# Kernel tuning notes

Measured on AMD Instinct MI355X. Metric: run time of the kernel, lower is better.

Reference implementation:

```python
import jax, jax.numpy as jnp
import numpy as np

FACTOR = 5      # ProbAttention sampling factor
NHEAD = 8
LN_EPS = 1e-5


def pos_encoding(L, d):
    pos = np.arange(L, dtype=np.float32)[:, None]
    div = np.exp(np.arange(0, d, 2, dtype=np.float32) * (-np.log(10000.0) / d))
    pe = np.zeros((L, d), np.float32)
    pe[:, 0::2] = np.sin(pos * div)
    pe[:, 1::2] = np.cos(pos * div)
    return jnp.asarray(pe)


def layer_norm(x, s, b):
    mu = x.mean(-1, keepdims=True)
    var = ((x - mu) ** 2).mean(-1, keepdims=True)
    return (x - mu) * jax.lax.rsqrt(var + LN_EPS) * s + b


def prob_attention(x4, key):
    # x4: [B, L, H, D]; self-attention (Q=K=V=x4), mask_flag=False
    B, L, H, D = x4.shape
    q = jnp.transpose(x4, (0, 2, 1, 3))  # [B,H,L,D]
    u = max(1, min(FACTOR * int(np.ceil(np.log(L))), L))  # L_Q == L_K
    # random K-sampling: per-query random subset of keys (shared across B,H)
    idx = jax.random.randint(key, (L, u), 0, L)
    k_s = q[:, :, idx, :]                                # [B,H,L,u,D] irregular gather
    qk_s = jnp.einsum('bhld,bhlsd->bhls', q, k_s)        # [B,H,L,u]
    M = qk_s.max(-1) - qk_s.sum(-1) / L                  # sparsity measure
    _, top = jax.lax.top_k(M, u)                         # [B,H,u] active queries
    q_red = jnp.take_along_axis(q, top[..., None], axis=2)   # [B,H,u,D]
    scale = 1.0 / jnp.sqrt(jnp.float32(D))
    scores = jnp.einsum('bhud,bhkd->bhuk', q_red, q) * scale  # reduced-query scores
    attn = jax.nn.softmax(scores, axis=-1)
    ctx_top = jnp.einsum('bhuk,bhkd->bhud', attn, q)     # V == q here
    # initial context = mean of V (mask_flag=False), scatter top-query results
    ctx = jnp.broadcast_to(q.mean(axis=2, keepdims=True), (B, H, L, D))
    bi = jnp.arange(B)[:, None, None]
    hi = jnp.arange(H)[None, :, None]
    ctx = ctx.at[bi, hi, top].set(ctx_top)
    return jnp.transpose(ctx, (0, 2, 1, 3))  # [B,L,H,D]


def encoder_layer(x4, ln1_s, ln1_b, w1, b1, w2, b2, ln2_s, ln2_b, key):
    B, L, H, D = x4.shape
    new = prob_attention(x4, key)
    x = x4.reshape(B, L, H * D)
    x = layer_norm(x + new.reshape(B, L, H * D), ln1_s, ln1_b)
    # conv1/conv2 with kernel_size=1 == pointwise linears
    y = jax.nn.gelu(jnp.einsum('bld,fd->blf', x, w1) + b1, approximate=False)
    y = jnp.einsum('blf,df->bld', y, w2) + b2
    x = layer_norm(x + y, ln2_s, ln2_b)
    return x.reshape(B, L, H, D)


def distil(x4, factor=2):
    # DistilledAttention: mean-pool over `factor` timesteps (zero-pad to multiple)
    B, L, H, D = x4.shape
    pad = (-L) % factor
    if pad:
        x4 = jnp.pad(x4, ((0, 0), (0, pad), (0, 0), (0, 0)))
    return x4.reshape(B, -1, factor, H, D).mean(axis=2)


def setup_inputs() -> dict:
    key = jax.random.key(0)
    B, L, IN, D, DF, NL = 8, 4096, 64, 512, 2048, 3
    ks = jax.random.split(key, 16)
    s = 0.02
    return {
        'x': jax.random.normal(ks[0], (B, L, IN), jnp.float32),
        'emb_w': jax.random.normal(ks[1], (D, IN), jnp.float32) * s,
        'emb_b': jnp.zeros((D,), jnp.float32),
        'ln1_s': jnp.ones((NL, D), jnp.float32),
        'ln1_b': jnp.zeros((NL, D), jnp.float32),
        'w1': jax.random.normal(ks[2], (NL, DF, D), jnp.float32) * s,
        'b1': jnp.zeros((NL, DF), jnp.float32),
        'w2': jax.random.normal(ks[3], (NL, D, DF), jnp.float32) * s,
        'b2': jnp.zeros((NL, D), jnp.float32),
        'ln2_s': jnp.ones((NL, D), jnp.float32),
        'ln2_b': jnp.zeros((NL, D), jnp.float32),
        'out_w': jax.random.normal(ks[4], (D, D), jnp.float32) * s,
        'out_b': jnp.zeros((D,), jnp.float32),
    }


def reference(x, emb_w, emb_b, ln1_s, ln1_b, w1, b1, w2, b2, ln2_s, ln2_b, out_w, out_b):
    B, L, _ = x.shape
    D = emb_w.shape[0]
    hd = D // NHEAD
    h = jnp.einsum('bli,di->bld', x, emb_w) + emb_b
    h = h + pos_encoding(L, D)[None]
    h = h.reshape(B, L, NHEAD, hd)
    NL = ln1_s.shape[0]
    rkey = jax.random.key(42)  # deterministic ProbSparse sampling
    for i in range(NL):
        h = encoder_layer(h, ln1_s[i], ln1_b[i], w1[i], b1[i], w2[i], b2[i],
                          ln2_s[i], ln2_b[i], jax.random.fold_in(rkey, i))
        if i < NL - 1:
            h = distil(h)
    B2, L2 = h.shape[:2]
    h = h.reshape(B2, L2, D)
    return jnp.einsum('bld,od->blo', h, out_w) + out_b
```

## Files before the change

### kernel.cpp

```cpp
#include <hip/hip_runtime.h>
#include <hip/hip_bf16.h>
#include <math.h>


typedef short short8 __attribute__((ext_vector_type(8)));
typedef float f32x4 __attribute__((ext_vector_type(4)));
typedef unsigned int uint;

__host__ __device__ inline void tf2x32(unsigned k0, unsigned k1,
                                       unsigned x0, unsigned x1,
                                       unsigned& o0, unsigned& o1) {
  unsigned ks2 = k0 ^ k1 ^ 0x1BD11BDAu;
#define TF_R(x, r) x0 += x1; x1 = ((x1 << (r)) | (x1 >> (32 - (r)))); x1 ^= x0;
  x0 += k0; x1 += k1;
  TF_R(x1,13) TF_R(x1,15) TF_R(x1,26) TF_R(x1,6)
  x0 += k1; x1 += ks2 + 1u;
  TF_R(x1,17) TF_R(x1,29) TF_R(x1,16) TF_R(x1,24)
  x0 += ks2; x1 += k0 + 2u;
  TF_R(x1,13) TF_R(x1,15) TF_R(x1,26) TF_R(x1,6)
  x0 += k0; x1 += k1 + 3u;
  TF_R(x1,17) TF_R(x1,29) TF_R(x1,16) TF_R(x1,24)
  x0 += k1; x1 += ks2 + 4u;
  TF_R(x1,13) TF_R(x1,15) TF_R(x1,26) TF_R(x1,6)
  x0 += ks2; x1 += k0 + 5u;
#undef TF_R
  o0 = x0; o1 = x1;
}

__global__ void k_idx(int* __restrict__ idx, unsigned k2a, unsigned k2b,
                      int n, int mask) {
  int j = blockIdx.x * 256 + threadIdx.x;
  if (j >= n) return;
  unsigned o0, o1;
  tf2x32(k2a, k2b, 0u, (unsigned)j, o0, o1);
  idx[j] = (int)((o0 ^ o1) & (unsigned)mask);
}

__global__ void k_pe(float* __restrict__ pe) {
  int t = blockIdx.x * 256 + threadIdx.x;
  int l = t >> 9, d = t & 511;
  double div = exp((double)(d & ~1) * (-9.210340371976184 / 512.0));
  double ang = (double)l * div;
  pe[t] = (float)((d & 1) ? cos(ang) : sin(ang));
}

__global__ __launch_bounds__(256) void k_embed(const float* __restrict__ x,
    const float* __restrict__ W, const float* __restrict__ eb,
    const float* __restrict__ pe, float* __restrict__ out) {
  __shared__ __align__(16) float xs[16][64];
  int r0 = blockIdx.x * 16;
  int t = threadIdx.x;
  ((float4*)&xs[0][0])[t] = ((const float4*)(x + (size_t)r0 * 64))[t];
  __syncthreads();
  int d0 = t, d1 = t + 256;
  float acc0[16], acc1[16];
#pragma unroll
  for (int r = 0; r < 16; r++) { acc0[r] = 0.f; acc1[r] = 0.f; }
  for (int k = 0; k < 64; k++) {
    float w0 = W[d0 * 64 + k], w1 = W[d1 * 64 + k];
#pragma unroll
    for (int r = 0; r < 16; r++) {
      float xv = xs[r][k];
      acc0[r] = fmaf(xv, w0, acc0[r]);
      acc1[r] = fmaf(xv, w1, acc1[r]);
    }
  }
  float eb0 = eb[d0], eb1 = eb[d1];
#pragma unroll
  for (int r = 0; r < 16; r++) {
    int row = r0 + r;
    int l = row & 4095;
    out[(size_t)row * 512 + d0] = acc0[r] + eb0 + pe[(size_t)l * 512 + d0];
    out[(size_t)row * 512 + d1] = acc1[r] + eb1 + pe[(size_t)l * 512 + d1];
  }
}

__global__ __launch_bounds__(256) void k_colmean1(const float* __restrict__ X,
    double* __restrict__ part, int L, int S) {
  int seg = blockIdx.x, bh = blockIdx.y, b = bh >> 3, h = bh & 7;
  int w = threadIdx.x >> 6, d = threadIdx.x & 63;
  int rows = L / S, r0 = seg * rows;
  const float* base = X + (size_t)b * L * 512 + h * 64 + d;
  double s = 0.0;
  for (int l = r0 + w; l < r0 + rows; l += 4) s += (double)base[(size_t)l * 512];
  __shared__ double red[4][64];
  red[w][d] = s;
  __syncthreads();
  if (w == 0)
    part[((size_t)bh * S + seg) * 64 + d] =
        red[0][d] + red[1][d] + red[2][d] + red[3][d];
}

__global__ void k_colmean2(const double* __restrict__ part,
    float* __restrict__ meanq, int L, int S) {
  int bh = blockIdx.x, d = threadIdx.x;
  const double* p = part + (size_t)bh * S * 64 + d;
  double s = 0.0;
  for (int seg = 0; seg < S; seg++) s += p[seg * 64];
  meanq[bh * 64 + d] = (float)(s / (double)L);
}

__global__ __launch_bounds__(256) void k_M(const float* __restrict__ X,
    const int* __restrict__ idx, float* __restrict__ Mout, int L, int Lsh,
    int u, float invL) {
  int w = threadIdx.x >> 6, lane = threadIdx.x & 63;
  int gl = blockIdx.x * 4 + w;
  int l = gl & (L - 1), bh = gl >> Lsh, b = bh >> 3, h = bh & 7;
  const float* Xbh = X + (size_t)b * L * 512 + h * 64;
  __shared__ float qs[4][64];
  qs[w][lane] = Xbh[(size_t)l * 512 + lane];
  __syncthreads();
  const int s16 = lane >> 2, j = lane & 3;
  float4 qv[4];
#pragma unroll
  for (int c = 0; c < 4; c++) qv[c] = *(const float4*)&qs[w][c * 16 + j * 4];
  const int base = l * u;
  int kx[3];
#pragma unroll
  for (int g = 0; g < 3; g++) {
    int s = g * 16 + s16;
    kx[g] = (s < u) ? idx[base + s] : 0;
  }
  float4 kv[3][4];
#pragma unroll
  for (int g = 0; g < 3; g++) {
    const float* row = Xbh + (size_t)kx[g] * 512 + j * 4;
#pragma unroll
    for (int c = 0; c < 4; c++) kv[g][c] = *(const float4*)(row + c * 16);
  }
  float mv = -1e30f, sv = 0.f;
#pragma unroll
  for (int g = 0; g < 3; g++) {
    float pc[4];
#pragma unroll
    for (int c = 0; c < 4; c++) {
      float p = qv[c].x * kv[g][c].x;
      p = fmaf(qv[c].y, kv[g][c].y, p);
      p = fmaf(qv[c].z, kv[g][c].z, p);
      p = fmaf(qv[c].w, kv[g][c].w, p);
      pc[c] = p;
    }
    float d = (pc[0] + pc[1]) + (pc[2] + pc[3]);
    d += __shfl_xor(d, 1);
    d += __shfl_xor(d, 2);
    if (g * 16 + s16 < u) { mv = fmaxf(mv, d); sv += d; }
  }
  for (int off = 4; off < 64; off <<= 1) {
    mv = fmaxf(mv, __shfl_xor(mv, off));
    sv += __shfl_xor(sv, off);
  }
  if (lane == 0) Mout[(size_t)bh * L + l] = mv - sv * invL;
}

__global__ __launch_bounds__(256) void k_topk(const float* __restrict__ M,
    int* __restrict__ top, int L, int u) {
  __shared__ float mv[4096];
  __shared__ float wv[4];
  __shared__ int wi[4];
  __shared__ int bi_s;
  int bh = blockIdx.x, t = threadIdx.x;
  int w = t >> 6, lane = t & 63;
  const float* Mr = M + (size_t)bh * L;
  for (int k = t; k < L; k += 256) mv[k] = Mr[k];
  __syncthreads();
  float lv = -1e30f; int li = 0x7fffffff;
  for (int k = t; k < L; k += 256) {
    float v = mv[k];
    if (v > lv) { lv = v; li = k; }
  }
  for (int it = 0; it < u; it++) {
    float v = lv; int i = li;
#pragma unroll
    for (int off = 1; off < 64; off <<= 1) {
      float v2 = __shfl_xor(v, off); int i2 = __shfl_xor(i, off);
      if (v2 > v || (v2 == v && i2 < i)) { v = v2; i = i2; }
    }
    if (lane == 0) { wv[w] = v; wi[w] = i; }
    __syncthreads();
    if (t == 0) {
      float bv = wv[0]; int bi = wi[0];
#pragma unroll
      for (int jj = 1; jj < 4; jj++) {
        if (wv[jj] > bv || (wv[jj] == bv && wi[jj] < bi)) { bv = wv[jj]; bi = wi[jj]; }
      }
      top[bh * u + it] = bi;
      mv[bi] = -1e30f;
      bi_s = bi;
    }
    __syncthreads();
    int bi = bi_s;
    if ((bi & 255) == t) {
      lv = -1e30f; li = 0x7fffffff;
      for (int k = t; k < L; k += 256) {
        float v = mv[k];
        if (v > lv) { lv = v; li = k; }
      }
    }
  }
}

__global__ __launch_bounds__(256) void k_scores(const float* __restrict__ X,
    const int* __restrict__ top, float* __restrict__ S, int L, int u) {
  __shared__ __align__(16) float ktT[64][68];
  __shared__ __align__(16) float qred[48][64];
  int bh = blockIdx.y, b = bh >> 3, h = bh & 7;
  int k0 = blockIdx.x * 64;
  int t = threadIdx.x;
  const float* Xbh = X + (size_t)b * L * 512 + h * 64;
#pragma unroll
  for (int it = 0; it < 4; it++) {
    int lin = t + it * 256;
    int kk = lin >> 4, fi = lin & 15;
    float4 v = *(const float4*)(Xbh + (size_t)(k0 + kk) * 512 + fi * 4);
    ktT[fi * 4 + 0][kk] = v.x; ktT[fi * 4 + 1][kk] = v.y;
    ktT[fi * 4 + 2][kk] = v.z; ktT[fi * 4 + 3][kk] = v.w;
  }
#pragma unroll
  for (int it = 0; it < 3; it++) {
    int lin = t + it * 256;
    int ur = lin >> 4, fi = lin & 15;
    if (ur < u) {
      int row = top[bh * u + ur];
      *(float4*)(&qred[ur][fi * 4]) = *(const float4*)(Xbh + (size_t)row * 512 + fi * 4);
    } else if (ur < 48) {
      *(float4*)(&qred[ur][fi * 4]) = make_float4(0.f, 0.f, 0.f, 0.f);
    }
  }
  __syncthreads();
  int xq = t & 15, y = t >> 4;
  float acc[3][4];
#pragma unroll
  for (int j = 0; j < 3; j++)
#pragma unroll
    for (int e = 0; e < 4; e++) acc[j][e] = 0.f;
  for (int d = 0; d < 64; d++) {
    float4 kv = *(const float4*)(&ktT[d][xq * 4]);
#pragma unroll
    for (int j = 0; j < 3; j++) {
      float qv = qred[y * 3 + j][d];
      acc[j][0] = fmaf(qv, kv.x, acc[j][0]);
      acc[j][1] = fmaf(qv, kv.y, acc[j][1]);
      acc[j][2] = fmaf(qv, kv.z, acc[j][2]);
      acc[j][3] = fmaf(qv, kv.w, acc[j][3]);
    }
  }
#pragma unroll
  for (int j = 0; j < 3; j++) {
    int ur = y * 3 + j;
    if (ur < u) {
      float4 o = make_float4(acc[j][0] * 0.125f, acc[j][1] * 0.125f,
                             acc[j][2] * 0.125f, acc[j][3] * 0.125f);
      *(float4*)(S + ((size_t)(bh * u + ur)) * L + k0 + xq * 4) = o;
    }
  }
}

__global__ __launch_bounds__(256) void k_smstat(const float* __restrict__ S,
    float* __restrict__ MX, double* __restrict__ INV, int L, int u) {
  int ur = blockIdx.x, bh = blockIdx.y;
  const float* Srow = S + ((size_t)(bh * u + ur)) * L;
  int t = threadIdx.x;
  __shared__ float rm[256];
  __shared__ double rs[256];
  float m = -1e30f;
  for (int k = t; k < L; k += 256) m = fmaxf(m, Srow[k]);
  rm[t] = m; __syncthreads();
  for (int off = 128; off; off >>= 1) {
    if (t < off) rm[t] = fmaxf(rm[t], rm[t + off]);
    __syncthreads();
  }
  float mx = rm[0];
  double s = 0.0;
  for (int k = t; k < L; k += 256) s += (double)expf(Srow[k] - mx);
  rs[t] = s; __syncthreads();
  for (int off = 128; off; off >>= 1) {
    if (t < off) rs[t] += rs[t + off];
    __syncthreads();
  }
  if (t == 0) { MX[bh * 48 + ur] = mx; INV[bh * 48 + ur] = 1.0 / rs[0]; }
}

#define PVSEG 8
__global__ __launch_bounds__(256) void k_pv(const float* __restrict__ X,
    const float* __restrict__ S, const float* __restrict__ MX,
    float* __restrict__ P2, int L, int u) {
  __shared__ __align__(16) float xs[32][64];
  __shared__ __align__(16) float wsm[32][52];
  int seg = blockIdx.x, bh = blockIdx.y, b = bh >> 3, h = bh & 7;
  int t = threadIdx.x, w = t >> 6, lane = t & 63;
  int rows = L / PVSEG, l0 = seg * rows;
  const float* Xb = X + (size_t)b * L * 512 + h * 64;
  int li = lane & 31, par = lane >> 5;
  const float* Sp[6]; float mxl[6]; int val[6];
#pragma unroll
  for (int jj = 0; jj < 6; jj++) {
    int ur = w * 12 + par + jj * 2;
    val[jj] = (ur < u);
    Sp[jj] = S + (size_t)(bh * u + (val[jj] ? ur : 0)) * L + l0 + li;
    mxl[jj] = val[jj] ? MX[bh * 48 + ur] : 0.f;
  }
  float acc[12];
#pragma unroll
  for (int j = 0; j < 12; j++) acc[j] = 0.f;
  int xr = t >> 4, xf = t & 15;
  for (int c = 0; c < rows; c += 32) {
    __syncthreads();
    *(float4*)&xs[xr][xf * 4] =
        *(const float4*)(Xb + (size_t)(l0 + c + xr) * 512 + xf * 4);
    *(float4*)&xs[16 + xr][xf * 4] =
        *(const float4*)(Xb + (size_t)(l0 + c + 16 + xr) * 512 + xf * 4);
#pragma unroll
    for (int jj = 0; jj < 6; jj++) {
      float e = val[jj] ? expf(Sp[jj][c] - mxl[jj]) : 0.f;
      wsm[li][w * 12 + par + jj * 2] = e;
    }
    __syncthreads();
#pragma unroll 2
    for (int l = 0; l < 32; l++) {
      float xv = xs[l][lane];
      float4 w0 = *(const float4*)&wsm[l][w * 12];
      float4 w1 = *(const float4*)&wsm[l][w * 12 + 4];
      float4 w2 = *(const float4*)&wsm[l][w * 12 + 8];
      acc[0]  = fmaf(w0.x, xv, acc[0]);  acc[1]  = fmaf(w0.y, xv, acc[1]);
      acc[2]  = fmaf(w0.z, xv, acc[2]);  acc[3]  = fmaf(w0.w, xv, acc[3]);
      acc[4]  = fmaf(w1.x, xv, acc[4]);  acc[5]  = fmaf(w1.y, xv, acc[5]);
      acc[6]  = fmaf(w1.z, xv, acc[6]);  acc[7]  = fmaf(w1.w, xv, acc[7]);
      acc[8]  = fmaf(w2.x, xv, acc[8]);  acc[9]  = fmaf(w2.y, xv, acc[9]);
      acc[10] = fmaf(w2.z, xv, acc[10]); acc[11] = fmaf(w2.w, xv, acc[11]);
    }
  }
  float* P = P2 + ((size_t)(bh * PVSEG + seg) * 48 + w * 12) * 64 + lane;
#pragma unroll
  for (int j = 0; j < 12; j++) P[j * 64] = acc[j];
}

__global__ __launch_bounds__(256) void k_pvred(const float* __restrict__ P2,
    const double* __restrict__ INV, const int* __restrict__ top,
    float* __restrict__ A, char* __restrict__ FLG, int L, int u) {
  int bh = blockIdx.x, b = bh >> 3, h = bh & 7;
  const float* Pb = P2 + (size_t)bh * PVSEG * 48 * 64;
  for (int e = threadIdx.x; e < u * 64; e += 256) {
    int ur = e >> 6, d = e & 63;
    const float* p = Pb + ur * 64 + d;
    const int st = 48 * 64;
    double s = ((double)p[0] + (double)p[st]) +
               ((double)p[2 * st] + (double)p[3 * st]) +
               ((double)p[4 * st] + (double)p[5 * st]) +
               ((double)p[6 * st] + (double)p[7 * st]);
    double tot = s * INV[bh * 48 + ur];
    int row = top[bh * u + ur];
    A[((size_t)b * L + row) * 512 + h * 64 + d] = (float)tot;
    if (d == 0) FLG[(size_t)bh * L + row] = 1;
  }
}

__global__ __launch_bounds__(256) void k_ln1(float* __restrict__ X,
    const float* __restrict__ A, const char* __restrict__ FLG,
    const float* __restrict__ meanq, const float* __restrict__ gs,
    const float* __restrict__ gb, int L, int Lsh) {
  int w = threadIdx.x >> 6, lane = threadIdx.x & 63;
  int row = blockIdx.x * 4 + w;
  int b = row >> Lsh, l = row & (L - 1);
  float* xr = X + (size_t)row * 512;
  const float* ar = A + (size_t)row * 512;
  const float* mq = meanq + b * 512;
  const char* fg = FLG + ((size_t)b * 8) * L + l;
  float v[8]; double s = 0.0, s2 = 0.0;
#pragma unroll
  for (int i = 0; i < 8; i++) {
    int d = lane + i * 64;
    float ctx = fg[(size_t)i * L] ? ar[d] : mq[d];
    float val = xr[d] + ctx;
    v[i] = val; s += (double)val; s2 += (double)val * (double)val;
  }
  for (int off = 32; off; off >>= 1) { s += __shfl_xor(s, off); s2 += __shfl_xor(s2, off); }
  double mu = s * (1.0 / 512.0);
  double var = s2 * (1.0 / 512.0) - mu * mu;
  float rsd = (float)(1.0 / sqrt(var + 1e-5));
  float muf = (float)mu;
#pragma unroll
  for (int i = 0; i < 8; i++) {
    int d = lane + i * 64;
    xr[d] = (v[i] - muf) * rsd * gs[d] + gb[d];
  }
}

__global__ __launch_bounds__(256) void k_ln2(const float* __restrict__ X,
    const float* __restrict__ Y2, const float* __restrict__ gs,
    const float* __restrict__ gb, float* __restrict__ out, int pool) {
  int w = threadIdx.x >> 6, lane = threadIdx.x & 63;
  int orow = blockIdx.x * 4 + w;
  float o[8] = {0.f,0.f,0.f,0.f,0.f,0.f,0.f,0.f};
  int reps = pool ? 2 : 1;
  for (int p = 0; p < reps; p++) {
    int row = pool ? (orow * 2 + p) : orow;
    const float* xr = X + (size_t)row * 512;
    const float* yr = Y2 + (size_t)row * 512;
    float v[8]; double s = 0.0, s2 = 0.0;
#pragma unroll
    for (int i = 0; i < 8; i++) {
      float val = xr[lane + i * 64] + yr[lane + i * 64];
      v[i] = val; s += (double)val; s2 += (double)val * (double)val;
    }
    for (int off = 32; off; off >>= 1) { s += __shfl_xor(s, off); s2 += __shfl_xor(s2, off); }
    double mu = s * (1.0 / 512.0);
    double var = s2 * (1.0 / 512.0) - mu * mu;
    float rsd = (float)(1.0 / sqrt(var + 1e-5));
    float muf = (float)mu;
#pragma unroll
    for (int i = 0; i < 8; i++)
      o[i] += (v[i] - muf) * rsd * gs[lane + i * 64] + gb[lane + i * 64];
  }
  float sc = pool ? 0.5f : 1.0f;
#pragma unroll
  for (int i = 0; i < 8; i++)
    out[(size_t)orow * 512 + lane + i * 64] = o[i] * sc;
}


__device__ inline unsigned bsplit(float x, float y, float& rx, float& ry) {
  union { __hip_bfloat162 h; unsigned u; } c;
  c.h = __float22bfloat162_rn(make_float2(x, y));
  rx = x - __uint_as_float(c.u << 16);
  ry = y - __uint_as_float(c.u & 0xffff0000u);
  return c.u;
}

__device__ inline void split2u(float4 v0, float4 v1, uint4& H, uint4& M) {
  float r[8]; float d0, d1;
  H.x = bsplit(v0.x, v0.y, r[0], r[1]);
  H.y = bsplit(v0.z, v0.w, r[2], r[3]);
  H.z = bsplit(v1.x, v1.y, r[4], r[5]);
  H.w = bsplit(v1.z, v1.w, r[6], r[7]);
  M.x = bsplit(r[0], r[1], d0, d1);
  M.y = bsplit(r[2], r[3], d0, d1);
  M.z = bsplit(r[4], r[5], d0, d1);
  M.w = bsplit(r[6], r[7], d0, d1);
}

__global__ void k_splitX(const float* __restrict__ X, char* __restrict__ P,
                         int K, int total8) {
  int f = blockIdx.x * 256 + threadIdx.x;
  if (f >= total8) return;
  int k8 = f % (K >> 3), m = f / (K >> 3);
  int k = k8 * 8;
  const float* src = X + (size_t)m * K + k;
  float4 v0 = *(const float4*)(src);
  float4 v1 = *(const float4*)(src + 4);
  uint4 H, Md;
  split2u(v0, v1, H, Md);
  size_t psz = (size_t)total8 * 16;
  size_t off = ((size_t)(m >> 4) * (K >> 5) + (k >> 5)) * 1024
             + (size_t)(((k >> 3) & 3) * 256 + (m & 15) * 16);
  *(uint4*)(P + off) = H;
  *(uint4*)(P + psz + off) = Md;
}

__device__ __forceinline__ void async16(void* lds, const void* g) {
  __builtin_amdgcn_global_load_lds(
      (const __attribute__((address_space(1))) uint*)g,
      (__attribute__((address_space(3))) uint*)lds, 16, 0, 0);
}

template <int MT, int GELU, int PLANES_OUT>
__global__ __launch_bounds__(256) void k_gemm6(const char* __restrict__ AP,
    const char* __restrict__ BP, const float* __restrict__ bias,
    void* __restrict__ Cout, int N, int K) {
  __shared__ __align__(16) char lds[(MT * 2 + 16) * 1024];
  const int t = threadIdx.x;
  const int w = t >> 6, lane = t & 63;
  const int bx = blockIdx.x, by = blockIdx.y;
  const int quad = lane >> 4, rit = lane & 15;
  const int Mrows = gridDim.y * (MT * 16);
  const size_t psA = (size_t)Mrows * K * 2;
  const size_t psB = (size_t)N * K * 2;
  const int KB = K >> 5;
  char* ldsA = lds;
  char* ldsB = lds + MT * 2 * 1024;
  const int wm = (w >> 1) * (MT / 2), wn = (w & 1) * 4;
  f32x4 acc[MT / 2][4];
#pragma unroll
  for (int i = 0; i < MT / 2; i++)
#pragma unroll
    for (int j = 0; j < 4; j++) acc[i][j] = (f32x4){0.f, 0.f, 0.f, 0.f};
  for (int kt = 0; kt < KB; kt++) {
#pragma unroll
    for (int r = 0; r < MT / 2; r++) {
      int q = w + 4 * r;
      int p = q / MT, tt = q % MT;
      async16(ldsA + (p * MT + tt) * 1024,
              AP + p * psA + ((size_t)(by * MT + tt) * KB + kt) * 1024 + lane * 16);
    }
#pragma unroll
    for (int r = 0; r < 4; r++) {
      int q = w + 4 * r;
      int p = q >> 3, tt = q & 7;
      async16(ldsB + (p * 8 + tt) * 1024,
              BP + p * psB + ((size_t)(bx * 8 + tt) * KB + kt) * 1024 + lane * 16);
    }
    __syncthreads();
    short8 af[2][MT / 2];
#pragma unroll
    for (int p = 0; p < 2; p++)
#pragma unroll
      for (int mi = 0; mi < MT / 2; mi++)
        af[p][mi] = *(const short8*)(ldsA + (p * MT + wm + mi) * 1024 + lane * 16);
#pragma unroll
    for (int ni = 0; ni < 4; ni++) {
      const char* bb = ldsB + (wn + ni) * 1024 + lane * 16;
      short8 bh = *(const short8*)(bb);
      short8 bm = *(const short8*)(bb + 8192);
#pragma unroll
      for (int mi = 0; mi < MT / 2; mi++) {
        f32x4 c = acc[mi][ni];
        c = __builtin_amdgcn_mfma_f32_16x16x32_bf16(af[0][mi], bh, c, 0, 0, 0);
        c = __builtin_amdgcn_mfma_f32_16x16x32_bf16(af[0][mi], bm, c, 0, 0, 0);
        c = __builtin_amdgcn_mfma_f32_16x16x32_bf16(af[1][mi], bh, c, 0, 0, 0);
        acc[mi][ni] = c;
      }
    }
    __syncthreads();
  }
  const int n0 = bx * 128, m_base = by * (MT * 16);
  if (!PLANES_OUT) {
    float* C = (float*)Cout;
#pragma unroll
    for (int mi = 0; mi < MT / 2; mi++) {
      const int gr0 = m_base + (wm + mi) * 16 + quad * 4;
#pragma unroll
      for (int ni = 0; ni < 4; ni++) {
        const int gc = n0 + (wn + ni) * 16 + rit;
        const float bia = bias[gc];
#pragma unroll
        for (int e = 0; e < 4; e++) {
          float v = acc[mi][ni][e] + bia;
          if (GELU) v = 0.5f * v * (1.0f + erff(v * 0.7071067811865476f));
          C[(size_t)(gr0 + e) * N + gc] = v;
        }
      }
    }
  } else {
    char* CP = (char*)Cout;
    const size_t psC = (size_t)Mrows * N * 2;
    float* lf = (float*)lds;
    for (int h = 0; h < 2; h++) {
      __syncthreads();
      if ((w & 1) == h) {
#pragma unroll
        for (int ni = 0; ni < 4; ni++) {
          const float bia = bias[n0 + h * 64 + ni * 16 + rit];
#pragma unroll
          for (int mi = 0; mi < MT / 2; mi++) {
            const int ml0 = (wm + mi) * 16 + quad * 4;
#pragma unroll
            for (int e = 0; e < 4; e++) {
              float v = acc[mi][ni][e] + bia;
              if (GELU) v = 0.5f * v * (1.0f + erff(v * 0.7071067811865476f));
              lf[(ml0 + e) * 64 + ni * 16 + rit] = v;
            }
          }
        }
      }
      __syncthreads();
#pragma unroll
      for (int it = 0; it < (MT * 16 * 8) / 256; it++) {
        int p = it * 256 + t;
        int ml = p >> 3, n8 = p & 7;
        float4 v0 = *(const float4*)&lf[ml * 64 + n8 * 8];
        float4 v1 = *(const float4*)&lf[ml * 64 + n8 * 8 + 4];
        uint4 H, Md;
        split2u(v0, v1, H, Md);
        int mg = m_base + ml, kg = n0 + h * 64 + n8 * 8;
        size_t off = ((size_t)(mg >> 4) * (N >> 5) + (kg >> 5)) * 1024
                   + (size_t)(((kg >> 3) & 3) * 256 + (mg & 15) * 16);
        *(uint4*)(CP + off) = H;
        *(uint4*)(CP + psC + off) = Md;
      }
    }
  }
}

extern "C" void kernel_launch(void* const* d_in, const int* in_sizes, int n_in,
                              void* d_out, int out_size, void* d_ws, size_t ws_size,
                              hipStream_t stream) {
  const float* x     = (const float*)d_in[0];
  const float* emb_w = (const float*)d_in[1];
  const float* emb_b = (const float*)d_in[2];
  const float* ln1_s = (const float*)d_in[3];
  const float* ln1_b = (const float*)d_in[4];
  const float* w1    = (const float*)d_in[5];
  const float* b1    = (const float*)d_in[6];
  const float* w2    = (const float*)d_in[7];
  const float* b2    = (const float*)d_in[8];
  const float* ln2_s = (const float*)d_in[9];
  const float* ln2_b = (const float*)d_in[10];
  const float* out_w = (const float*)d_in[11];
  const float* out_b = (const float*)d_in[12];
  float* outp = (float*)d_out;

  char* ws = (char*)d_ws;
  if (ws_size < (212ULL << 20)) return;
  float* PE    = (float*)(ws);
  char*  W1S   = ws;
  float* BUF[3] = { (float*)(ws + (8ULL << 20)),
                    (float*)(ws + (72ULL << 20)),
                    (float*)(ws + (136ULL << 20)) };
  char*  W2S   = ws + (200ULL << 20);
  float* MB    = (float*)(ws + (206ULL << 20));
  int*   IDX   = (int*)  (ws + (207ULL << 20));
  int*   TOP   = (int*)  (ws + (208ULL << 20));
  float* MEANQ = (float*)(ws + (208ULL << 20) + (64 << 10));
  float* MXB   = (float*)(ws + (208ULL << 20) + (128 << 10));
  double* INVB = (double*)(ws + (208ULL << 20) + (192 << 10));
  double* PART = (double*)(ws + (209ULL << 20));
  char*  FLG   = ws + (210ULL << 20);

  k_pe<<<4096 * 512 / 256, 256, 0, stream>>>(PE);
  k_embed<<<(8 * 4096) / 16, 256, 0, stream>>>(x, emb_w, emb_b, PE, BUF[0]);

  const int Ls[3] = {4096, 2048, 1024};
  const int Lshs[3] = {12, 11, 10};
  const int us[3] = {45, 40, 35};
  int xi = 0, ai = 1, yi = 2;
  for (int layer = 0; layer < 3; layer++) {
    const int L = Ls[layer], u = us[layer];
    float* X = BUF[xi]; float* A = BUF[ai]; float* Y = BUF[yi];

    k_splitX<<<(2048 * 512 / 8) / 256, 256, 0, stream>>>(
        w1 + (size_t)layer * 2048 * 512, W1S, 512, 2048 * 512 / 8);
    k_splitX<<<(512 * 2048 / 8) / 256, 256, 0, stream>>>(
        w2 + (size_t)layer * 512 * 2048, W2S, 2048, 512 * 2048 / 8);

    unsigned Ka, Kb, k2a, k2b;
    tf2x32(0u, 42u, 0u, (unsigned)layer, Ka, Kb);
    tf2x32(Ka, Kb, 0u, 1u, k2a, k2b);
    const int n = L * u;
    k_idx<<<(n + 255) / 256, 256, 0, stream>>>(IDX, k2a, k2b, n, L - 1);
    const int S = 32;
    k_colmean1<<<dim3(S, 64), 256, 0, stream>>>(X, PART, L, S);
    k_colmean2<<<64, 64, 0, stream>>>(PART, MEANQ, L, S);
    k_M<<<64 * L / 4, 256, 0, stream>>>(X, IDX, MB, L, Lshs[layer], u,
                                        1.0f / (float)L);
    k_topk<<<64, 256, 0, stream>>>(MB, TOP, L, u);
    hipMemsetAsync(FLG, 0, (size_t)64 * L, stream);
    k_scores<<<dim3(L / 64, 64), 256, 0, stream>>>(X, TOP, Y, L, u);
    float* P2 = (float*)((char*)Y + (48ULL << 20));
    k_smstat<<<dim3(u, 64), 256, 0, stream>>>(Y, MXB, INVB, L, u);
    k_pv<<<dim3(PVSEG, 64), 256, 0, stream>>>(X, Y, MXB, P2, L, u);
    k_pvred<<<64, 256, 0, stream>>>(P2, INVB, TOP, A, FLG, L, u);
    k_ln1<<<8 * L / 4, 256, 0, stream>>>(X, A, FLG, MEANQ,
                                         ln1_s + layer * 512,
                                         ln1_b + layer * 512, L, Lshs[layer]);

    char* YP = (char*)Y;
    const int chunks = (8 * L) / 8192;
    for (int c = 0; c < chunks; c++) {
      const float* Xc = X + (size_t)c * 8192 * 512;
      float* Ac = A + (size_t)c * 8192 * 512;
      char* XP = (char*)Ac;
      k_splitX<<<(8192 * 512 / 8) / 256, 256, 0, stream>>>(
          Xc, XP, 512, 8192 * 512 / 8);
      k_gemm6<8, 1, 1><<<dim3(16, 64), 256, 0, stream>>>(
          XP, W1S, b1 + layer * 2048, YP, 2048, 512);
      k_gemm6<4, 0, 0><<<dim3(4, 128), 256, 0, stream>>>(
          YP, W2S, b2 + layer * 512, Ac, 512, 2048);
    }
    if (layer < 2)
      k_ln2<<<8 * (L / 2) / 4, 256, 0, stream>>>(X, A, ln2_s + layer * 512,
                                                 ln2_b + layer * 512, Y, 1);
    else
      k_ln2<<<8 * L / 4, 256, 0, stream>>>(X, A, ln2_s + layer * 512,
                                           ln2_b + layer * 512, Y, 0);
    int tswap = xi; xi = yi; yi = ai; ai = tswap;
  }
  char* XFP = (char*)BUF[ai];
  char* WOS = W2S;
  k_splitX<<<(512 * 512 / 8) / 256, 256, 0, stream>>>(out_w, WOS, 512, 512 * 512 / 8);
  k_splitX<<<(8192 * 512 / 8) / 256, 256, 0, stream>>>(BUF[xi], XFP, 512, 8192 * 512 / 8);
  k_gemm6<4, 0, 0><<<dim3(4, 128), 256, 0, stream>>>(
      XFP, WOS, out_b, outp, 512, 512);
}
```

Measured before the change: 2.215 ms.

## Fuse bf16 split packing into LayerNorm kernels and compact attention context

The bf16 hi/lo split-and-pack of the LN1 output is folded into k_ln1, which now writes the GEMM operand layout directly, so the per-chunk k_splitX pass over X goes away. The final layer's LN2 gets a new k_ln2p kernel that writes packed operands for the output projection, dropping one more split pass. k_pvred now writes a compact per-head context buffer and stores the top-query slot in FLG, and LN1 reads that with vectorized float4 loads. A __syncthreads in k_M is removed, which relies on each wave reading only the shared row it wrote itself.

```diff
diff --git a/kernel.cpp b/kernel.cpp
--- a/kernel.cpp
+++ b/kernel.cpp
@@ -27,6 +27,27 @@
   o0 = x0; o1 = x1;
 }
 
+
+__device__ inline unsigned bsplit(float x, float y, float& rx, float& ry) {
+  union { __hip_bfloat162 h; unsigned u; } c;
+  c.h = __float22bfloat162_rn(make_float2(x, y));
+  rx = x - __uint_as_float(c.u << 16);
+  ry = y - __uint_as_float(c.u & 0xffff0000u);
+  return c.u;
+}
+
+__device__ inline void split2u(float4 v0, float4 v1, uint4& H, uint4& M) {
+  float r[8]; float d0, d1;
+  H.x = bsplit(v0.x, v0.y, r[0], r[1]);
+  H.y = bsplit(v0.z, v0.w, r[2], r[3]);
+  H.z = bsplit(v1.x, v1.y, r[4], r[5]);
+  H.w = bsplit(v1.z, v1.w, r[6], r[7]);
+  M.x = bsplit(r[0], r[1], d0, d1);
+  M.y = bsplit(r[2], r[3], d0, d1);
+  M.z = bsplit(r[4], r[5], d0, d1);
+  M.w = bsplit(r[6], r[7], d0, d1);
+}
+
 __global__ void k_idx(int* __restrict__ idx, unsigned k2a, unsigned k2b,
                       int n, int mask) {
   int j = blockIdx.x * 256 + threadIdx.x;
@@ -109,7 +130,6 @@
   const float* Xbh = X + (size_t)b * L * 512 + h * 64;
   __shared__ float qs[4][64];
   qs[w][lane] = Xbh[(size_t)l * 512 + lane];
-  __syncthreads();
   const int s16 = lane >> 2, j = lane & 3;
   float4 qv[4];
 #pragma unroll
@@ -336,8 +356,8 @@
 
 __global__ __launch_bounds__(256) void k_pvred(const float* __restrict__ P2,
     const double* __restrict__ INV, const int* __restrict__ top,
-    float* __restrict__ A, char* __restrict__ FLG, int L, int u) {
-  int bh = blockIdx.x, b = bh >> 3, h = bh & 7;
+    float* __restrict__ CTX, char* __restrict__ FLG, int L, int u) {
+  int bh = blockIdx.x;
   const float* Pb = P2 + (size_t)bh * PVSEG * 48 * 64;
   for (int e = threadIdx.x; e < u * 64; e += 256) {
     int ur = e >> 6, d = e & 63;
@@ -348,52 +368,76 @@
                ((double)p[4 * st] + (double)p[5 * st]) +
                ((double)p[6 * st] + (double)p[7 * st]);
     double tot = s * INV[bh * 48 + ur];
-    int row = top[bh * u + ur];
-    A[((size_t)b * L + row) * 512 + h * 64 + d] = (float)tot;
-    if (d == 0) FLG[(size_t)bh * L + row] = 1;
+    CTX[((size_t)bh * 48 + ur) * 64 + d] = (float)tot;
+    if (d == 0) FLG[(size_t)bh * L + top[bh * u + ur]] = (char)(ur + 1);
   }
 }
 
 __global__ __launch_bounds__(256) void k_ln1(float* __restrict__ X,
-    const float* __restrict__ A, const char* __restrict__ FLG,
+    const char* __restrict__ FLG, const float* __restrict__ CTX,
     const float* __restrict__ meanq, const float* __restrict__ gs,
-    const float* __restrict__ gb, int L, int Lsh) {
+    const float* __restrict__ gb, char* __restrict__ XPbase, int L, int Lsh) {
   int w = threadIdx.x >> 6, lane = threadIdx.x & 63;
   int row = blockIdx.x * 4 + w;
   int b = row >> Lsh, l = row & (L - 1);
   float* xr = X + (size_t)row * 512;
-  const float* ar = A + (size_t)row * 512;
-  const float* mq = meanq + b * 512;
-  const char* fg = FLG + ((size_t)b * 8) * L + l;
-  float v[8]; double s = 0.0, s2 = 0.0;
-#pragma unroll
-  for (int i = 0; i < 8; i++) {
-    int d = lane + i * 64;
-    float ctx = fg[(size_t)i * L] ? ar[d] : mq[d];
-    float val = xr[d] + ctx;
-    v[i] = val; s += (double)val; s2 += (double)val * (double)val;
-  }
+  int h = lane >> 3;
+  int bh = b * 8 + h;
+  int flag = (int)FLG[(size_t)bh * L + l];
+  float4 c0, c1;
+  if (flag) {
+    const float* cx = CTX + ((size_t)bh * 48 + (flag - 1)) * 64 + (lane & 7) * 8;
+    c0 = *(const float4*)cx; c1 = *(const float4*)(cx + 4);
+  } else {
+    const float* mq = meanq + b * 512 + lane * 8;
+    c0 = *(const float4*)mq; c1 = *(const float4*)(mq + 4);
+  }
+  float4 x0 = *(const float4*)(xr + lane * 8);
+  float4 x1 = *(const float4*)(xr + lane * 8 + 4);
+  float v[8] = { x0.x + c0.x, x0.y + c0.y, x0.z + c0.z, x0.w + c0.w,
+                 x1.x + c1.x, x1.y + c1.y, x1.z + c1.z, x1.w + c1.w };
+  double s = 0.0, s2 = 0.0;
+#pragma unroll
+  for (int i = 0; i < 8; i++) { s += (double)v[i]; s2 += (double)v[i] * (double)v[i]; }
   for (int off = 32; off; off >>= 1) { s += __shfl_xor(s, off); s2 += __shfl_xor(s2, off); }
   double mu = s * (1.0 / 512.0);
   double var = s2 * (1.0 / 512.0) - mu * mu;
   float rsd = (float)(1.0 / sqrt(var + 1e-5));
   float muf = (float)mu;
-#pragma unroll
-  for (int i = 0; i < 8; i++) {
-    int d = lane + i * 64;
-    xr[d] = (v[i] - muf) * rsd * gs[d] + gb[d];
-  }
+  float4 g0 = *(const float4*)(gs + lane * 8);
+  float4 g1 = *(const float4*)(gs + lane * 8 + 4);
+  float4 b0 = *(const float4*)(gb + lane * 8);
+  float4 b1 = *(const float4*)(gb + lane * 8 + 4);
+  float4 y0 = make_float4((v[0] - muf) * rsd * g0.x + b0.x,
+                          (v[1] - muf) * rsd * g0.y + b0.y,
+                          (v[2] - muf) * rsd * g0.z + b0.z,
+                          (v[3] - muf) * rsd * g0.w + b0.w);
+  float4 y1 = make_float4((v[4] - muf) * rsd * g1.x + b1.x,
+                          (v[5] - muf) * rsd * g1.y + b1.y,
+                          (v[6] - muf) * rsd * g1.z + b1.z,
+                          (v[7] - muf) * rsd * g1.w + b1.w);
+  *(float4*)(xr + lane * 8) = y0;
+  *(float4*)(xr + lane * 8 + 4) = y1;
+  int c = row >> 13, ml = row & 8191;
+  char* P = XPbase + ((size_t)c << 24);
+  const size_t psz = (size_t)8192 * 512 * 2;
+  int k = lane * 8;
+  size_t off = ((size_t)(ml >> 4) * 16 + (k >> 5)) * 1024
+             + (size_t)(((k >> 3) & 3) * 256 + (ml & 15) * 16);
+  uint4 H, Md;
+  split2u(y0, y1, H, Md);
+  *(uint4*)(P + off) = H;
+  *(uint4*)(P + psz + off) = Md;
 }
 
 __global__ __launch_bounds__(256) void k_ln2(const float* __restrict__ X,
     const float* __restrict__ Y2, const float* __restrict__ gs,
-    const float* __restrict__ gb, float* __restrict__ out, int pool) {
+    const float* __restrict__ gb, float* __restrict__ out) {
   int w = threadIdx.x >> 6, lane = threadIdx.x & 63;
   int orow = blockIdx.x * 4 + w;
   float o[8] = {0.f,0.f,0.f,0.f,0.f,0.f,0.f,0.f};
-  int reps = pool ? 2 : 1;
-  for (int p = 0; p < reps; p++) {
-    int row = pool ? (orow * 2 + p) : orow;
+  for (int p = 0; p < 2; p++) {
+    int row = orow * 2 + p;
     const float* xr = X + (size_t)row * 512;
     const float* yr = Y2 + (size_t)row * 512;
     float v[8]; double s = 0.0, s2 = 0.0;
@@ -411,31 +455,52 @@
     for (int i = 0; i < 8; i++)
       o[i] += (v[i] - muf) * rsd * gs[lane + i * 64] + gb[lane + i * 64];
   }
-  float sc = pool ? 0.5f : 1.0f;
 #pragma unroll
   for (int i = 0; i < 8; i++)
-    out[(size_t)orow * 512 + lane + i * 64] = o[i] * sc;
-}
-
-
-__device__ inline unsigned bsplit(float x, float y, float& rx, float& ry) {
-  union { __hip_bfloat162 h; unsigned u; } c;
-  c.h = __float22bfloat162_rn(make_float2(x, y));
-  rx = x - __uint_as_float(c.u << 16);
-  ry = y - __uint_as_float(c.u & 0xffff0000u);
-  return c.u;
-}
-
-__device__ inline void split2u(float4 v0, float4 v1, uint4& H, uint4& M) {
-  float r[8]; float d0, d1;
-  H.x = bsplit(v0.x, v0.y, r[0], r[1]);
-  H.y = bsplit(v0.z, v0.w, r[2], r[3]);
-  H.z = bsplit(v1.x, v1.y, r[4], r[5]);
-  H.w = bsplit(v1.z, v1.w, r[6], r[7]);
-  M.x = bsplit(r[0], r[1], d0, d1);
-  M.y = bsplit(r[2], r[3], d0, d1);
-  M.z = bsplit(r[4], r[5], d0, d1);
-  M.w = bsplit(r[6], r[7], d0, d1);
+    out[(size_t)orow * 512 + lane + i * 64] = o[i] * 0.5f;
+}
+
+__global__ __launch_bounds__(256) void k_ln2p(const float* __restrict__ X,
+    const float* __restrict__ Y2, const float* __restrict__ gs,
+    const float* __restrict__ gb, char* __restrict__ P) {
+  int w = threadIdx.x >> 6, lane = threadIdx.x & 63;
+  int row = blockIdx.x * 4 + w;
+  const float* xr = X + (size_t)row * 512;
+  const float* yr = Y2 + (size_t)row * 512;
+  float4 x0 = *(const float4*)(xr + lane * 8);
+  float4 x1 = *(const float4*)(xr + lane * 8 + 4);
+  float4 z0 = *(const float4*)(yr + lane * 8);
+  float4 z1 = *(const float4*)(yr + lane * 8 + 4);
+  float v[8] = { x0.x + z0.x, x0.y + z0.y, x0.z + z0.z, x0.w + z0.w,
+                 x1.x + z1.x, x1.y + z1.y, x1.z + z1.z, x1.w + z1.w };
+  double s = 0.0, s2 = 0.0;
+#pragma unroll
+  for (int i = 0; i < 8; i++) { s += (double)v[i]; s2 += (double)v[i] * (double)v[i]; }
+  for (int off = 32; off; off >>= 1) { s += __shfl_xor(s, off); s2 += __shfl_xor(s2, off); }
+  double mu = s * (1.0 / 512.0);
+  double var = s2 * (1.0 / 512.0) - mu * mu;
+  float rsd = (float)(1.0 / sqrt(var + 1e-5));
+  float muf = (float)mu;
+  float4 g0 = *(const float4*)(gs + lane * 8);
+  float4 g1 = *(const float4*)(gs + lane * 8 + 4);
+  float4 b0 = *(const float4*)(gb + lane * 8);
+  float4 b1 = *(const float4*)(gb + lane * 8 + 4);
+  float4 y0 = make_float4((v[0] - muf) * rsd * g0.x + b0.x,
+                          (v[1] - muf) * rsd * g0.y + b0.y,
+                          (v[2] - muf) * rsd * g0.z + b0.z,
+                          (v[3] - muf) * rsd * g0.w + b0.w);
+  float4 y1 = make_float4((v[4] - muf) * rsd * g1.x + b1.x,
+                          (v[5] - muf) * rsd * g1.y + b1.y,
+                          (v[6] - muf) * rsd * g1.z + b1.z,
+                          (v[7] - muf) * rsd * g1.w + b1.w);
+  const size_t psz = (size_t)8192 * 512 * 2;
+  int k = lane * 8;
+  size_t off = ((size_t)(row >> 4) * 16 + (k >> 5)) * 1024
+             + (size_t)(((k >> 3) & 3) * 256 + (row & 15) * 16);
+  uint4 H, Md;
+  split2u(y0, y1, H, Md);
+  *(uint4*)(P + off) = H;
+  *(uint4*)(P + psz + off) = Md;
 }
 
 __global__ void k_splitX(const float* __restrict__ X, char* __restrict__ P,
@@ -614,6 +679,7 @@
   double* INVB = (double*)(ws + (208ULL << 20) + (192 << 10));
   double* PART = (double*)(ws + (209ULL << 20));
   char*  FLG   = ws + (210ULL << 20);
+  float* CTX   = (float*)(ws + (210ULL << 20) + (512 << 10));
 
   k_pe<<<4096 * 512 / 256, 256, 0, stream>>>(PE);
   k_embed<<<(8 * 4096) / 16, 256, 0, stream>>>(x, emb_w, emb_b, PE, BUF[0]);
@@ -622,6 +688,7 @@
   const int Lshs[3] = {12, 11, 10};
   const int us[3] = {45, 40, 35};
   int xi = 0, ai = 1, yi = 2;
+  char* FINALP = nullptr;
   for (int layer = 0; layer < 3; layer++) {
     const int L = Ls[layer], u = us[layer];
     float* X = BUF[xi]; float* A = BUF[ai]; float* Y = BUF[yi];
@@ -647,36 +714,34 @@
     float* P2 = (float*)((char*)Y + (48ULL << 20));
     k_smstat<<<dim3(u, 64), 256, 0, stream>>>(Y, MXB, INVB, L, u);
     k_pv<<<dim3(PVSEG, 64), 256, 0, stream>>>(X, Y, MXB, P2, L, u);
-    k_pvred<<<64, 256, 0, stream>>>(P2, INVB, TOP, A, FLG, L, u);
-    k_ln1<<<8 * L / 4, 256, 0, stream>>>(X, A, FLG, MEANQ,
+    k_pvred<<<64, 256, 0, stream>>>(P2, INVB, TOP, CTX, FLG, L, u);
+    k_ln1<<<8 * L / 4, 256, 0, stream>>>(X, FLG, CTX, MEANQ,
                                          ln1_s + layer * 512,
-                                         ln1_b + layer * 512, L, Lshs[layer]);
+                                         ln1_b + layer * 512, (char*)A,
+                                         L, Lshs[layer]);
 
     char* YP = (char*)Y;
     const int chunks = (8 * L) / 8192;
     for (int c = 0; c < chunks; c++) {
-      const float* Xc = X + (size_t)c * 8192 * 512;
       float* Ac = A + (size_t)c * 8192 * 512;
       char* XP = (char*)Ac;
-      k_splitX<<<(8192 * 512 / 8) / 256, 256, 0, stream>>>(
-          Xc, XP, 512, 8192 * 512 / 8);
       k_gemm6<8, 1, 1><<<dim3(16, 64), 256, 0, stream>>>(
           XP, W1S, b1 + layer * 2048, YP, 2048, 512);
       k_gemm6<4, 0, 0><<<dim3(4, 128), 256, 0, stream>>>(
           YP, W2S, b2 + layer * 512, Ac, 512, 2048);
     }
-    if (layer < 2)
+    if (layer < 2) {
       k_ln2<<<8 * (L / 2) / 4, 256, 0, stream>>>(X, A, ln2_s + layer * 512,
-                                                 ln2_b + layer * 512, Y, 1);
-    else
-      k_ln2<<<8 * L / 4, 256, 0, stream>>>(X, A, ln2_s + layer * 512,
-                                           ln2_b + layer * 512, Y, 0);
+                                                 ln2_b + layer * 512, Y);
+    } else {
+      FINALP = (char*)Y;
+      k_ln2p<<<8 * L / 4, 256, 0, stream>>>(X, A, ln2_s + layer * 512,
+                                            ln2_b + layer * 512, FINALP);
+    }
     int tswap = xi; xi = yi; yi = ai; ai = tswap;
   }
-  char* XFP = (char*)BUF[ai];
   char* WOS = W2S;
   k_splitX<<<(512 * 512 / 8) / 256, 256, 0, stream>>>(out_w, WOS, 512, 512 * 512 / 8);
-  k_splitX<<<(8192 * 512 / 8) / 256, 256, 0, stream>>>(BUF[xi], XFP, 512, 8192 * 512 / 8);
   k_gemm6<4, 0, 0><<<dim3(4, 128), 256, 0, stream>>>(
-      XFP, WOS, out_b, outp, 512, 512);
-}
+      FINALP, WOS, out_b, outp, 512, 512);
+}
```

Result: no change. 2.182 ms (-1.5%).
